# Performance work log

Hardware: AMD Instinct MI355X
Metric: run time of the kernel (lower is better)

The kernel has to match this reference:

```python
import math
import jax, jax.numpy as jnp
import numpy as np

H = 16  # head_count

def setup_inputs() -> dict:
    key = jax.random.key(0)
    ks = jax.random.split(key, 7)
    B, S, D = 2, 2048, 1024
    query = jax.random.normal(ks[0], (B, S, D), dtype=jnp.float32)
    # mask: True = masked position (matches masked_fill_ semantics)
    mask = jax.random.randint(ks[1], (B, S, S), 0, 2) > 0
    scale = 1.0 / math.sqrt(D)  # xavier-ish init scale
    Wq = jax.random.normal(ks[2], (D, D), dtype=jnp.float32) * scale
    Wk = jax.random.normal(ks[3], (D, D), dtype=jnp.float32) * scale
    Wv = jax.random.normal(ks[4], (D, D), dtype=jnp.float32) * scale
    Wo = jax.random.normal(ks[5], (D, D), dtype=jnp.float32) * scale
    bo = jnp.zeros((D,), dtype=jnp.float32)
    return {"query": query, "mask": mask, "Wq": Wq, "Wk": Wk, "Wv": Wv, "Wo": Wo, "bo": bo}


def reference(query, mask, Wq, Wk, Wv, Wo, bo):
    B, S, D = query.shape
    dh = D // H

    def split_heads(x):  # [B,S,D] -> [B,H,S,dh]
        return x.reshape(B, S, H, dh).transpose(0, 2, 1, 3)

    # torch nn.Linear computes x @ W.T (bias-free for q/k/v)
    q = split_heads(query @ Wq.T) * (1.0 / math.sqrt(dh))
    k = split_heads(query @ Wk.T)
    v = split_heads(query @ Wv.T)

    scores = jnp.einsum('bhqd,bhkd->bhqk', q, k)           # [B,H,S,S]
    scores = jnp.where(mask[:, None, :, :], jnp.float32(-1e18), scores)
    weights = jax.nn.softmax(scores, axis=-1)               # dropout=0 -> identity
    ctx = jnp.einsum('bhqk,bhkd->bhqd', weights, v)         # [B,H,S,dh]
    ctx = ctx.transpose(0, 2, 1, 3).reshape(B, S, D)        # combine heads
    return ctx @ Wo.T + bo
```

## Files before the change

### kernel.cpp

```cpp
#include <hip/hip_runtime.h>

#define S_LEN 2048
#define D_MODEL 1024
#define NH 16
#define DH 64

typedef __bf16 bf16x8 __attribute__((ext_vector_type(8)));
typedef __bf16 bf16x4 __attribute__((ext_vector_type(4)));
typedef float f32x4 __attribute__((ext_vector_type(4)));

__device__ __forceinline__ unsigned short f2bf(float f) {
  unsigned int x = __float_as_uint(f);
  x += 0x7fffu + ((x >> 16) & 1u);
  return (unsigned short)(x >> 16);
}

__device__ __forceinline__ bf16x4 cvt4(f32x4 v) {
  return __builtin_convertvector(v, bf16x4);
}

__device__ __forceinline__ float exp2raw(float x) {
#if __has_builtin(__builtin_amdgcn_exp2f)
  return __builtin_amdgcn_exp2f(x);
#else
  return exp2f(x);
#endif
}

__device__ __forceinline__ f32x4 mfma16(bf16x8 a, bf16x8 b, f32x4 c) {
  return __builtin_amdgcn_mfma_f32_16x16x32_bf16(a, b, c, 0, 0, 0);
}

__device__ __forceinline__ void gl2lds(const unsigned short* g, unsigned short* l) {
  __builtin_amdgcn_global_load_lds(
      (__attribute__((address_space(1))) void*)g,
      (__attribute__((address_space(3))) void*)l, 16, 0, 0);
}

__global__ __launch_bounds__(256) void prep_kernel(
    const float* __restrict__ q, const float* __restrict__ wq,
    const float* __restrict__ wk, const float* __restrict__ wv,
    const float* __restrict__ wo, const int* __restrict__ mask,
    unsigned short* __restrict__ qbf, unsigned short* __restrict__ wbf,
    unsigned long long* __restrict__ bits) {
  const int bx = blockIdx.x;
  if (bx < 32768) {
    int i = bx * 256 + threadIdx.x;
    unsigned long long bal = __ballot(mask[i] != 0);
    if ((threadIdx.x & 63) == 0) bits[i >> 6] = bal;
  } else {
    const long t = (long)(bx - 32768) * 256 + threadIdx.x;
    const float* src;
    unsigned short* dst;
    long e;
    if (t < 524288) { src = q; dst = qbf; e = t * 8; }
    else {
      long u = t - 524288;
      int wi = (int)(u >> 17);
      e = (u & 131071) * 8;
      src = wi == 0 ? wq : wi == 1 ? wk : wi == 2 ? wv : wo;
      dst = wbf + (long)wi * 1048576;
    }
    float4 a = *(const float4*)(src + e);
    float4 b = *(const float4*)(src + e + 4);
    ushort4 p0 = {f2bf(a.x), f2bf(a.y), f2bf(a.z), f2bf(a.w)};
    ushort4 p1 = {f2bf(b.x), f2bf(b.y), f2bf(b.z), f2bf(b.w)};
    *(ushort4*)(dst + e) = p0;
    *(ushort4*)(dst + e + 4) = p1;
  }
}

__global__ __launch_bounds__(256) void gemm_qkv(
    const unsigned short* __restrict__ A, const unsigned short* __restrict__ W3,
    unsigned short* __restrict__ qb, unsigned short* __restrict__ kb,
    unsigned short* __restrict__ vt, float qscale) {
  __shared__ unsigned short As[128 * 64];
  __shared__ unsigned short Bs[128 * 64];
  const int tid = threadIdx.x, lane = tid & 63, wid = tid >> 6;
  const int wm = wid >> 1, wn = wid & 1;
  const int quad = lane >> 4, c = lane & 15, cx = c & 7;
  const int nG = blockIdx.x * 128;
  const int wi = nG >> 10, nn0 = nG & 1023;
  const int m0 = blockIdx.y * 128;
  const unsigned short* Bsrc = W3 + (size_t)wi * 1048576;
  const int srow = lane >> 3;
  const int schk = ((lane & 7) ^ srow) * 8;
  const unsigned short* ag = A + (size_t)(m0 + wid * 32 + srow) * 1024 + schk;
  const unsigned short* bg = Bsrc + (size_t)(nn0 + wid * 32 + srow) * 1024 + schk;
  f32x4 acc[4][4] = {};
  for (int kk = 0; kk < 1024; kk += 64) {
#pragma unroll
    for (int i = 0; i < 4; ++i) {
      gl2lds(ag + (size_t)(i * 8) * 1024 + kk, &As[(wid * 32 + i * 8) * 64]);
      gl2lds(bg + (size_t)(i * 8) * 1024 + kk, &Bs[(wid * 32 + i * 8) * 64]);
    }
    __syncthreads();
#pragma unroll
    for (int kc = 0; kc < 2; ++kc) {
      bf16x8 a[4], b[4];
#pragma unroll
      for (int mt = 0; mt < 4; ++mt)
        a[mt] = *(const bf16x8*)(
            &As[(wm * 64 + mt * 16 + c) * 64 + ((kc * 4 + quad) ^ cx) * 8]);
#pragma unroll
      for (int nt = 0; nt < 4; ++nt)
        b[nt] = *(const bf16x8*)(
            &Bs[(wn * 64 + nt * 16 + c) * 64 + ((kc * 4 + quad) ^ cx) * 8]);
#pragma unroll
      for (int mt = 0; mt < 4; ++mt)
#pragma unroll
        for (int nt = 0; nt < 4; ++nt)
          acc[mt][nt] = mfma16(a[mt], b[nt], acc[mt][nt]);
    }
    __syncthreads();
  }
#pragma unroll
  for (int mt = 0; mt < 4; ++mt) {
#pragma unroll
    for (int nt = 0; nt < 4; ++nt) {
      const int mb = m0 + wm * 64 + mt * 16 + quad * 4;
      const int n = nn0 + wn * 64 + nt * 16 + c;
      const int hh = n >> 6, d = n & 63;
      const int bb = mb >> 11, ss = mb & 2047;
      if (wi == 0) {
#pragma unroll
        for (int r = 0; r < 4; ++r)
          qb[(size_t)((bb * NH + hh) * S_LEN + ss + r) * DH + d] =
              f2bf(acc[mt][nt][r] * qscale);
      } else if (wi == 1) {
#pragma unroll
        for (int r = 0; r < 4; ++r)
          kb[(size_t)((bb * NH + hh) * S_LEN + ss + r) * DH + d] =
              f2bf(acc[mt][nt][r]);
      } else {
        *(bf16x4*)(vt + (size_t)((bb * NH + hh) * DH + d) * S_LEN + ss) =
            cvt4(acc[mt][nt]);
      }
    }
  }
}

__global__ __launch_bounds__(256) void gemm_out(
    const unsigned short* __restrict__ A, const unsigned short* __restrict__ W,
    float* __restrict__ out, const float* __restrict__ bias) {
  __shared__ unsigned short As[128 * 64];
  __shared__ unsigned short Bs[64 * 64];
  const int tid = threadIdx.x, lane = tid & 63, wid = tid >> 6;
  const int wm = wid >> 1, wn = wid & 1;
  const int quad = lane >> 4, c = lane & 15, cx = c & 7;
  const int n0 = blockIdx.x * 64, m0 = blockIdx.y * 128;
  const int srow = lane >> 3;
  const int schk = ((lane & 7) ^ srow) * 8;
  const unsigned short* ag = A + (size_t)(m0 + wid * 32 + srow) * 1024 + schk;
  const unsigned short* bg = W + (size_t)(n0 + wid * 16 + srow) * 1024 + schk;
  f32x4 acc[4][2] = {};
  for (int kk = 0; kk < 1024; kk += 64) {
#pragma unroll
    for (int i = 0; i < 4; ++i)
      gl2lds(ag + (size_t)(i * 8) * 1024 + kk, &As[(wid * 32 + i * 8) * 64]);
#pragma unroll
    for (int i = 0; i < 2; ++i)
      gl2lds(bg + (size_t)(i * 8) * 1024 + kk, &Bs[(wid * 16 + i * 8) * 64]);
    __syncthreads();
#pragma unroll
    for (int kc = 0; kc < 2; ++kc) {
      bf16x8 a[4], b[2];
#pragma unroll
      for (int mt = 0; mt < 4; ++mt)
        a[mt] = *(const bf16x8*)(
            &As[(wm * 64 + mt * 16 + c) * 64 + ((kc * 4 + quad) ^ cx) * 8]);
#pragma unroll
      for (int nt = 0; nt < 2; ++nt)
        b[nt] = *(const bf16x8*)(
            &Bs[(wn * 32 + nt * 16 + c) * 64 + ((kc * 4 + quad) ^ cx) * 8]);
#pragma unroll
      for (int mt = 0; mt < 4; ++mt)
#pragma unroll
        for (int nt = 0; nt < 2; ++nt)
          acc[mt][nt] = mfma16(a[mt], b[nt], acc[mt][nt]);
    }
    __syncthreads();
  }
#pragma unroll
  for (int mt = 0; mt < 4; ++mt) {
#pragma unroll
    for (int nt = 0; nt < 2; ++nt) {
      const int mb = m0 + wm * 64 + mt * 16 + quad * 4;
      const int n = n0 + wn * 32 + nt * 16 + c;
      const float bv = bias[n];
#pragma unroll
      for (int r = 0; r < 4; ++r)
        out[(size_t)(mb + r) * D_MODEL + n] = acc[mt][nt][r] + bv;
    }
  }
}

__global__ __launch_bounds__(256, 2) void attn_kernel(
    const unsigned short* __restrict__ qb, const unsigned short* __restrict__ kb,
    const unsigned short* __restrict__ vt,
    const unsigned long long* __restrict__ mbits,
    unsigned short* __restrict__ ctx) {
  const int h = blockIdx.x, qt = blockIdx.y, b = blockIdx.z;
  const int bh = b * NH + h;
  const int tid = threadIdx.x, lane = tid & 63, wid = tid >> 6;
  const int quad = lane >> 4, c = lane & 15, cx = c & 7;
  const int qw = wid & 1, kh = wid >> 1;
  const int q0 = qt * 128;
  __shared__ __align__(16) unsigned short KV[4][4096];
  __shared__ __align__(16) unsigned short Pbuf[4][64 * 72];

  const int qbase = q0 + qw * 64;
  const unsigned short* qp = qb + (size_t)(bh * S_LEN + qbase + c) * DH;
  bf16x8 bq[4][2];
#pragma unroll
  for (int sub = 0; sub < 4; ++sub) {
    bq[sub][0] = *(const bf16x8*)(qp + sub * 16 * DH + quad * 8);
    bq[sub][1] = *(const bf16x8*)(qp + sub * 16 * DH + 32 + quad * 8);
  }

  f32x4 o[4][4] = {};
  float lacc[4] = {0.f, 0.f, 0.f, 0.f};
  const unsigned long long* mq0 =
      mbits + (size_t)(b * S_LEN + qbase + c) * 32 + kh * 16;

  const int srow = lane >> 3, schk = ((lane & 7) ^ srow) * 8;
  const unsigned short* Ksh = KV[kh];
  const unsigned short* Vsh = KV[2 + kh];
  unsigned short* Pw = Pbuf[wid];

  const unsigned short* gK =
      kb + (size_t)(bh * S_LEN + (wid & 1) * 1024 + srow) * DH + schk;
  const unsigned short* gV =
      vt + (size_t)(bh * DH + srow) * S_LEN + (wid - 2) * 1024 + schk;

  for (int kt = 0; kt < 1024; kt += 64) {
    if (wid < 2) {
#pragma unroll
      for (int i = 0; i < 8; ++i)
        gl2lds(gK + (size_t)(kt + i * 8) * DH, &KV[wid][i * 512]);
    } else {
#pragma unroll
      for (int i = 0; i < 8; ++i)
        gl2lds(gV + (size_t)(i * 8) * S_LEN + kt, &KV[wid][i * 512]);
    }
    __syncthreads();

    bf16x8 kf[8];
#pragma unroll
    for (int g = 0; g < 4; ++g) {
      const int rho = g * 16 + c;
      kf[2 * g] = *(const bf16x8*)(&Ksh[rho * 64 + (quad ^ cx) * 8]);
      kf[2 * g + 1] = *(const bf16x8*)(&Ksh[rho * 64 + ((4 + quad) ^ cx) * 8]);
    }

    const int mi = kt >> 6;
#pragma unroll
    for (int sub = 0; sub < 4; ++sub) {
      f32x4 s[4];
#pragma unroll
      for (int g = 0; g < 4; ++g) {
        f32x4 z = {};
        z = mfma16(kf[2 * g], bq[sub][0], z);
        z = mfma16(kf[2 * g + 1], bq[sub][1], z);
        s[g] = z;
      }
      const unsigned long long w64 = mq0[sub * 512 + mi];
      const unsigned int wlo = (unsigned int)w64;
      const unsigned int whi = (unsigned int)(w64 >> 32);
      float lp = 0.f;
#pragma unroll
      for (int g = 0; g < 4; ++g) {
        const unsigned int bits =
            ((g & 2) ? whi : wlo) >> ((g & 1) * 16 + quad * 4);
        f32x4 p;
#pragma unroll
        for (int r = 0; r < 4; ++r) {
          const float e = exp2raw(s[g][r]);
          p[r] = ((bits >> r) & 1u) ? 0.f : e;
          lp += p[r];
        }
        *(bf16x4*)(&Pw[(sub * 16 + c) * 72 + g * 16 + quad * 4]) = cvt4(p);
      }
      lacc[sub] += lp;
    }

#pragma unroll
    for (int ks = 0; ks < 2; ++ks) {
      bf16x8 bp[4];
#pragma unroll
      for (int sub = 0; sub < 4; ++sub)
        bp[sub] =
            *(const bf16x8*)(&Pw[(sub * 16 + c) * 72 + ks * 32 + quad * 8]);
#pragma unroll
      for (int nt = 0; nt < 4; ++nt) {
        bf16x8 av = *(const bf16x8*)(
            &Vsh[(nt * 16 + c) * 64 + ((ks * 4 + quad) ^ cx) * 8]);
#pragma unroll
        for (int sub = 0; sub < 4; ++sub)
          o[sub][nt] = mfma16(av, bp[sub], o[sub][nt]);
      }
    }
    __syncthreads();
  }

#pragma unroll
  for (int sub = 0; sub < 4; ++sub) {
    lacc[sub] += __shfl_xor(lacc[sub], 16, 64);
    lacc[sub] += __shfl_xor(lacc[sub], 32, 64);
  }

  float* mrg = (float*)&Pbuf[0][0];
  float* ml = mrg + 8 * 1088;
  if (kh == 1) {
#pragma unroll
    for (int sub = 0; sub < 4; ++sub) {
      float* mo = mrg + (qw * 4 + sub) * 1088;
#pragma unroll
      for (int nt = 0; nt < 4; ++nt)
        *(f32x4*)(mo + c * 68 + nt * 16 + quad * 4) = o[sub][nt];
      if (quad == 0) ml[(qw * 4 + sub) * 16 + c] = lacc[sub];
    }
  }
  __syncthreads();
  if (kh == 0) {
#pragma unroll
    for (int sub = 0; sub < 4; ++sub) {
      const int pp = qw * 4 + sub;
      const float inv = 1.0f / (lacc[sub] + ml[pp * 16 + c]);
      const int q = qbase + sub * 16 + c;
      const float* mo = mrg + pp * 1088;
#pragma unroll
      for (int nt = 0; nt < 4; ++nt) {
        f32x4 ob = *(const f32x4*)(mo + c * 68 + nt * 16 + quad * 4);
        f32x4 rr = (o[sub][nt] + ob) * inv;
        *(bf16x4*)(ctx + (size_t)(b * S_LEN + q) * D_MODEL + h * DH + nt * 16 +
                   quad * 4) = cvt4(rr);
      }
    }
  }
}

extern "C" void kernel_launch(void* const* d_in, const int* in_sizes, int n_in,
                              void* d_out, int out_size, void* d_ws, size_t ws_size,
                              hipStream_t stream) {
  const float* query = (const float*)d_in[0];
  const int* mask = (const int*)d_in[1];
  const float* Wq = (const float*)d_in[2];
  const float* Wk = (const float*)d_in[3];
  const float* Wv = (const float*)d_in[4];
  const float* Wo = (const float*)d_in[5];
  const float* bo = (const float*)d_in[6];
  float* out = (float*)d_out;

  char* ws = (char*)d_ws;
  const size_t MB = 1024 * 1024;
  unsigned short* qbf = (unsigned short*)(ws);
  unsigned short* wbf = (unsigned short*)(ws + 8 * MB);
  unsigned short* qb = (unsigned short*)(ws + 16 * MB);
  unsigned short* kb = (unsigned short*)(ws + 24 * MB);
  unsigned short* vt = (unsigned short*)(ws + 32 * MB);
  unsigned long long* mb = (unsigned long long*)(ws + 40 * MB);
  unsigned short* ctx = qbf;

  prep_kernel<<<32768 + 4096, 256, 0, stream>>>(query, Wq, Wk, Wv, Wo, mask,
                                                qbf, wbf, mb);

  gemm_qkv<<<dim3(3072 / 128, 4096 / 128), 256, 0, stream>>>(
      qbf, wbf, qb, kb, vt, 0.18033688f);

  attn_kernel<<<dim3(NH, S_LEN / 128, 2), 256, 0, stream>>>(qb, kb, vt, mb,
                                                            ctx);

  gemm_out<<<dim3(1024 / 64, 4096 / 128), 256, 0, stream>>>(
      ctx, wbf + 3 * 1048576, out, bo);
}
```

Measured before the change: 222.9 us.

## Split attention keys across four waves and read K/V directly from global

The attention kernel stops staging K and V tiles in shared memory with barriers. Each of the four waves now owns 64 queries and a quarter of the key range, loading K and V fragments straight from global memory. The query tile per block shrinks to 64, which doubles the grid and raises launch bounds to 4 blocks per SM. Partial outputs and row sums from the four waves are combined through shared memory in two stages. This removes per-tile barriers and LDS traffic, but gives up sharing K/V through LDS, so global/L2 traffic rises and load latency is no longer hidden by the staged copies.

```diff
diff --git a/kernel.cpp b/kernel.cpp
--- a/kernel.cpp
+++ b/kernel.cpp
@@ -195,22 +195,19 @@
   }
 }
 
-__global__ __launch_bounds__(256, 2) void attn_kernel(
+__global__ __launch_bounds__(256, 4) void attn_kernel(
     const unsigned short* __restrict__ qb, const unsigned short* __restrict__ kb,
     const unsigned short* __restrict__ vt,
     const unsigned long long* __restrict__ mbits,
     unsigned short* __restrict__ ctx) {
   const int h = blockIdx.x, qt = blockIdx.y, b = blockIdx.z;
   const int bh = b * NH + h;
-  const int tid = threadIdx.x, lane = tid & 63, wid = tid >> 6;
-  const int quad = lane >> 4, c = lane & 15, cx = c & 7;
-  const int qw = wid & 1, kh = wid >> 1;
-  const int q0 = qt * 128;
-  __shared__ __align__(16) unsigned short KV[4][4096];
+  const int tid = threadIdx.x, lane = tid & 63, kh = tid >> 6;
+  const int quad = lane >> 4, c = lane & 15;
+  const int q0 = qt * 64;
   __shared__ __align__(16) unsigned short Pbuf[4][64 * 72];
 
-  const int qbase = q0 + qw * 64;
-  const unsigned short* qp = qb + (size_t)(bh * S_LEN + qbase + c) * DH;
+  const unsigned short* qp = qb + (size_t)(bh * S_LEN + q0 + c) * DH;
   bf16x8 bq[4][2];
 #pragma unroll
   for (int sub = 0; sub < 4; ++sub) {
@@ -221,39 +218,21 @@
   f32x4 o[4][4] = {};
   float lacc[4] = {0.f, 0.f, 0.f, 0.f};
   const unsigned long long* mq0 =
-      mbits + (size_t)(b * S_LEN + qbase + c) * 32 + kh * 16;
-
-  const int srow = lane >> 3, schk = ((lane & 7) ^ srow) * 8;
-  const unsigned short* Ksh = KV[kh];
-  const unsigned short* Vsh = KV[2 + kh];
-  unsigned short* Pw = Pbuf[wid];
-
-  const unsigned short* gK =
-      kb + (size_t)(bh * S_LEN + (wid & 1) * 1024 + srow) * DH + schk;
-  const unsigned short* gV =
-      vt + (size_t)(bh * DH + srow) * S_LEN + (wid - 2) * 1024 + schk;
-
-  for (int kt = 0; kt < 1024; kt += 64) {
-    if (wid < 2) {
-#pragma unroll
-      for (int i = 0; i < 8; ++i)
-        gl2lds(gK + (size_t)(kt + i * 8) * DH, &KV[wid][i * 512]);
-    } else {
-#pragma unroll
-      for (int i = 0; i < 8; ++i)
-        gl2lds(gV + (size_t)(i * 8) * S_LEN + kt, &KV[wid][i * 512]);
-    }
-    __syncthreads();
-
+      mbits + (size_t)(b * S_LEN + q0 + c) * 32 + kh * 8;
+  const unsigned short* gK = kb + (size_t)(bh * S_LEN + kh * 512) * DH;
+  const unsigned short* gV = vt + (size_t)bh * DH * S_LEN + kh * 512;
+  unsigned short* Pw = Pbuf[kh];
+
+  for (int t = 0; t < 8; ++t) {
+    const int kt = t * 64;
     bf16x8 kf[8];
 #pragma unroll
     for (int g = 0; g < 4; ++g) {
-      const int rho = g * 16 + c;
-      kf[2 * g] = *(const bf16x8*)(&Ksh[rho * 64 + (quad ^ cx) * 8]);
-      kf[2 * g + 1] = *(const bf16x8*)(&Ksh[rho * 64 + ((4 + quad) ^ cx) * 8]);
-    }
-
-    const int mi = kt >> 6;
+      const unsigned short* kr = gK + (size_t)(kt + g * 16 + c) * DH + quad * 8;
+      kf[2 * g] = *(const bf16x8*)(kr);
+      kf[2 * g + 1] = *(const bf16x8*)(kr + 32);
+    }
+
 #pragma unroll
     for (int sub = 0; sub < 4; ++sub) {
       f32x4 s[4];
@@ -264,7 +243,7 @@
         z = mfma16(kf[2 * g + 1], bq[sub][1], z);
         s[g] = z;
       }
-      const unsigned long long w64 = mq0[sub * 512 + mi];
+      const unsigned long long w64 = mq0[sub * 512 + t];
       const unsigned int wlo = (unsigned int)w64;
       const unsigned int whi = (unsigned int)(w64 >> 32);
       float lp = 0.f;
@@ -294,13 +273,12 @@
 #pragma unroll
       for (int nt = 0; nt < 4; ++nt) {
         bf16x8 av = *(const bf16x8*)(
-            &Vsh[(nt * 16 + c) * 64 + ((ks * 4 + quad) ^ cx) * 8]);
+            gV + (size_t)(nt * 16 + c) * S_LEN + kt + ks * 32 + quad * 8);
 #pragma unroll
         for (int sub = 0; sub < 4; ++sub)
           o[sub][nt] = mfma16(av, bp[sub], o[sub][nt]);
       }
     }
-    __syncthreads();
   }
 
 #pragma unroll
@@ -310,29 +288,51 @@
   }
 
   float* mrg = (float*)&Pbuf[0][0];
-  float* ml = mrg + 8 * 1088;
+  float* ml = mrg + 2 * 4352;
+  __syncthreads();
+  if (kh >= 2) {
+    float* mo = mrg + (kh - 2) * 4352;
+#pragma unroll
+    for (int sub = 0; sub < 4; ++sub) {
+#pragma unroll
+      for (int nt = 0; nt < 4; ++nt)
+        *(f32x4*)(mo + sub * 1088 + c * 68 + nt * 16 + quad * 4) = o[sub][nt];
+      if (quad == 0) ml[(kh - 2) * 64 + sub * 16 + c] = lacc[sub];
+    }
+  }
+  __syncthreads();
+  if (kh < 2) {
+    const float* mo = mrg + kh * 4352;
+#pragma unroll
+    for (int sub = 0; sub < 4; ++sub) {
+#pragma unroll
+      for (int nt = 0; nt < 4; ++nt)
+        o[sub][nt] +=
+            *(const f32x4*)(mo + sub * 1088 + c * 68 + nt * 16 + quad * 4);
+      lacc[sub] += ml[kh * 64 + sub * 16 + c];
+    }
+  }
+  __syncthreads();
   if (kh == 1) {
 #pragma unroll
     for (int sub = 0; sub < 4; ++sub) {
-      float* mo = mrg + (qw * 4 + sub) * 1088;
 #pragma unroll
       for (int nt = 0; nt < 4; ++nt)
-        *(f32x4*)(mo + c * 68 + nt * 16 + quad * 4) = o[sub][nt];
-      if (quad == 0) ml[(qw * 4 + sub) * 16 + c] = lacc[sub];
+        *(f32x4*)(mrg + sub * 1088 + c * 68 + nt * 16 + quad * 4) = o[sub][nt];
+      if (quad == 0) ml[sub * 16 + c] = lacc[sub];
     }
   }
   __syncthreads();
   if (kh == 0) {
 #pragma unroll
     for (int sub = 0; sub < 4; ++sub) {
-      const int pp = qw * 4 + sub;
-      const float inv = 1.0f / (lacc[sub] + ml[pp * 16 + c]);
-      const int q = qbase + sub * 16 + c;
-      const float* mo = mrg + pp * 1088;
+      const float linv = 1.0f / (lacc[sub] + ml[sub * 16 + c]);
+      const int q = q0 + sub * 16 + c;
 #pragma unroll
       for (int nt = 0; nt < 4; ++nt) {
-        f32x4 ob = *(const f32x4*)(mo + c * 68 + nt * 16 + quad * 4);
-        f32x4 rr = (o[sub][nt] + ob) * inv;
+        f32x4 ob =
+            *(const f32x4*)(mrg + sub * 1088 + c * 68 + nt * 16 + quad * 4);
+        f32x4 rr = (o[sub][nt] + ob) * linv;
         *(bf16x4*)(ctx + (size_t)(b * S_LEN + q) * D_MODEL + h * DH + nt * 16 +
                    quad * 4) = cvt4(rr);
       }
@@ -368,8 +368,8 @@
   gemm_qkv<<<dim3(3072 / 128, 4096 / 128), 256, 0, stream>>>(
       qbf, wbf, qb, kb, vt, 0.18033688f);
 
-  attn_kernel<<<dim3(NH, S_LEN / 128, 2), 256, 0, stream>>>(qb, kb, vt, mb,
-                                                            ctx);
+  attn_kernel<<<dim3(NH, S_LEN / 64, 2), 256, 0, stream>>>(qb, kb, vt, mb,
+                                                           ctx);
 
   gemm_out<<<dim3(1024 / 64, 4096 / 128), 256, 0, stream>>>(
       ctx, wbf + 3 * 1048576, out, bo);
```

After: 352.8 us. 58.3% more time.

## Keep softmax probabilities in registers by permuting K rows, dropping the P LDS roundtrip

Applied to the files above, without the earlier changes.

K rows are loaded into shared memory in a permuted order, so the MFMA output layout of the score tile lines up with the B-operand layout the PV MFMA needs. The probabilities are packed directly into bf16x8 registers instead of being written to and re-read from a per-wave LDS buffer. The mask bit indexing is changed to match the permutation. Shared memory is merged into one smaller buffer, which may allow higher occupancy, but register pressure rises from holding the packed P fragments.

```diff
diff --git a/kernel.cpp b/kernel.cpp
--- a/kernel.cpp
+++ b/kernel.cpp
@@ -206,8 +206,8 @@
   const int quad = lane >> 4, c = lane & 15, cx = c & 7;
   const int qw = wid & 1, kh = wid >> 1;
   const int q0 = qt * 128;
-  __shared__ __align__(16) unsigned short KV[4][4096];
-  __shared__ __align__(16) unsigned short Pbuf[4][64 * 72];
+  __shared__ __align__(16) char smem[35328];
+  unsigned short* KVb = (unsigned short*)smem;
 
   const int qbase = q0 + qw * 64;
   const unsigned short* qp = qb + (size_t)(bh * S_LEN + qbase + c) * DH;
@@ -224,24 +224,26 @@
       mbits + (size_t)(b * S_LEN + qbase + c) * 32 + kh * 16;
 
   const int srow = lane >> 3, schk = ((lane & 7) ^ srow) * 8;
-  const unsigned short* Ksh = KV[kh];
-  const unsigned short* Vsh = KV[2 + kh];
-  unsigned short* Pw = Pbuf[wid];
-
-  const unsigned short* gK =
-      kb + (size_t)(bh * S_LEN + (wid & 1) * 1024 + srow) * DH + schk;
+  const unsigned short* Ksh = KVb + kh * 4096;
+  const unsigned short* Vsh = KVb + (2 + kh) * 4096;
+
+  const unsigned short* gKb =
+      kb + (size_t)(bh * S_LEN + (wid & 1) * 1024) * DH + schk;
   const unsigned short* gV =
       vt + (size_t)(bh * DH + srow) * S_LEN + (wid - 2) * 1024 + schk;
 
   for (int kt = 0; kt < 1024; kt += 64) {
     if (wid < 2) {
 #pragma unroll
+      for (int i = 0; i < 8; ++i) {
+        const int t = i * 8 + srow;
+        const int st = (t & 0x23) | ((t >> 2) & 0x04) | ((t << 1) & 0x18);
+        gl2lds(gKb + (size_t)(kt + st) * DH, &KVb[wid * 4096 + i * 512]);
+      }
+    } else {
+#pragma unroll
       for (int i = 0; i < 8; ++i)
-        gl2lds(gK + (size_t)(kt + i * 8) * DH, &KV[wid][i * 512]);
-    } else {
-#pragma unroll
-      for (int i = 0; i < 8; ++i)
-        gl2lds(gV + (size_t)(i * 8) * S_LEN + kt, &KV[wid][i * 512]);
+        gl2lds(gV + (size_t)(i * 8) * S_LEN + kt, &KVb[wid * 4096 + i * 512]);
     }
     __syncthreads();
 
@@ -254,6 +256,7 @@
     }
 
     const int mi = kt >> 6;
+    bf16x8 bps[4][2];
 #pragma unroll
     for (int sub = 0; sub < 4; ++sub) {
       f32x4 s[4];
@@ -268,36 +271,35 @@
       const unsigned int wlo = (unsigned int)w64;
       const unsigned int whi = (unsigned int)(w64 >> 32);
       float lp = 0.f;
+      f32x4 p[4];
 #pragma unroll
       for (int g = 0; g < 4; ++g) {
         const unsigned int bits =
-            ((g & 2) ? whi : wlo) >> ((g & 1) * 16 + quad * 4);
-        f32x4 p;
+            ((g & 2) ? whi : wlo) >> (quad * 8 + (g & 1) * 4);
 #pragma unroll
         for (int r = 0; r < 4; ++r) {
           const float e = exp2raw(s[g][r]);
-          p[r] = ((bits >> r) & 1u) ? 0.f : e;
-          lp += p[r];
+          p[g][r] = ((bits >> r) & 1u) ? 0.f : e;
+          lp += p[g][r];
         }
-        *(bf16x4*)(&Pw[(sub * 16 + c) * 72 + g * 16 + quad * 4]) = cvt4(p);
-      }
+      }
+      union { bf16x8 v; bf16x4 h[2]; } u0, u1;
+      u0.h[0] = cvt4(p[0]); u0.h[1] = cvt4(p[1]);
+      u1.h[0] = cvt4(p[2]); u1.h[1] = cvt4(p[3]);
+      bps[sub][0] = u0.v;
+      bps[sub][1] = u1.v;
       lacc[sub] += lp;
     }
 
 #pragma unroll
     for (int ks = 0; ks < 2; ++ks) {
-      bf16x8 bp[4];
-#pragma unroll
-      for (int sub = 0; sub < 4; ++sub)
-        bp[sub] =
-            *(const bf16x8*)(&Pw[(sub * 16 + c) * 72 + ks * 32 + quad * 8]);
 #pragma unroll
       for (int nt = 0; nt < 4; ++nt) {
         bf16x8 av = *(const bf16x8*)(
             &Vsh[(nt * 16 + c) * 64 + ((ks * 4 + quad) ^ cx) * 8]);
 #pragma unroll
         for (int sub = 0; sub < 4; ++sub)
-          o[sub][nt] = mfma16(av, bp[sub], o[sub][nt]);
+          o[sub][nt] = mfma16(av, bps[sub][ks], o[sub][nt]);
       }
     }
     __syncthreads();
@@ -309,7 +311,7 @@
     lacc[sub] += __shfl_xor(lacc[sub], 32, 64);
   }
 
-  float* mrg = (float*)&Pbuf[0][0];
+  float* mrg = (float*)smem;
   float* ml = mrg + 8 * 1088;
   if (kh == 1) {
 #pragma unroll
```

After: 222.0 us. No clear change (-0.4%).
